# Performance work log

Measured on AMD Instinct MI355X. Metric: run time of the kernel, lower is better.

The kernel has to match this reference:

```python
import jax, jax.numpy as jnp
import numpy as np

N_NODES = 100000
N_EDGES = 1000000
IN_F, HID_F, OUT_F = 128, 128, 16


def setup_inputs() -> dict:
    key = jax.random.key(0)
    ks = jax.random.split(key, 8)
    x = jax.random.normal(ks[0], (N_NODES, IN_F), dtype=jnp.float32)
    src = jax.random.randint(ks[1], (N_EDGES,), 0, N_NODES, dtype=jnp.int64)
    dst = jax.random.randint(ks[2], (N_EDGES,), 0, N_NODES, dtype=jnp.int64)
    s = 1.0 / np.sqrt(HID_F)
    W1 = jax.random.normal(ks[3], (IN_F, HID_F), dtype=jnp.float32) * s
    W2 = jax.random.normal(ks[4], (HID_F, HID_F), dtype=jnp.float32) * s
    W3 = jax.random.normal(ks[5], (HID_F, HID_F), dtype=jnp.float32) * s
    W4 = jax.random.normal(ks[6], (HID_F, HID_F), dtype=jnp.float32) * s
    W5 = jax.random.normal(ks[7], (HID_F, OUT_F), dtype=jnp.float32) * s
    return {
        "x": x, "src": src, "dst": dst,
        "W1": W1, "b1": jnp.zeros((HID_F,), jnp.float32),
        "W2": W2, "b2": jnp.zeros((HID_F,), jnp.float32),
        "W3": W3, "b3": jnp.zeros((HID_F,), jnp.float32),
        "W4": W4, "b4": jnp.zeros((HID_F,), jnp.float32),
        "W5": W5, "b5": jnp.zeros((OUT_F,), jnp.float32),
    }


def reference(x, src, dst, W1, b1, W2, b2, W3, b3, W4, b4, W5, b5):
    N = x.shape[0]
    # in-degree per destination node (static graph, computed once)
    deg = jax.ops.segment_sum(jnp.ones_like(dst, dtype=x.dtype), dst, num_segments=N)
    inv = (1.0 / (deg + 1.0))[:, None]  # gcn aggregator normalizer: 1/(deg_in+1)

    def sage_gcn(h, W, b):
        # h_neigh[v] = (h[v] + sum_{u->v} h[u]) / (deg_in(v)+1); then linear
        agg = (h + jax.ops.segment_sum(h[src], dst, num_segments=N)) * inv
        return agg @ W + b

    h = jax.nn.relu(sage_gcn(x, W1, b1))
    h = jax.nn.relu(sage_gcn(h, W2, b2))
    h = jax.nn.relu(sage_gcn(h, W3, b3))
    h = jax.nn.relu(sage_gcn(h, W4, b4))
    h = sage_gcn(h, W5, b5)
    return jax.nn.log_softmax(h, axis=-1)
```

## Files before the change

kernel.cpp:

```cpp
#include <hip/hip_runtime.h>
#include <hip/hip_bf16.h>

#define NNODES 100000
#define NP (NNODES + 8)
#define NEDGES 1000000
#define HID 128
#define OUTF 16
#define NB 16
#define NBKT (NNODES / NB)
#define BCAP 81920
#define KB 64
#define BZT 1024
#define NSL 4

typedef __attribute__((ext_vector_type(8))) short short8;
typedef __attribute__((ext_vector_type(4))) float floatx4;
typedef __attribute__((ext_vector_type(4))) unsigned int uintx4;
typedef unsigned int uint32;
typedef unsigned long long ull;
typedef unsigned short ushort16;

__device__ __forceinline__ float blo(uint32 u) { return __uint_as_float(u << 16); }
__device__ __forceinline__ float bhi(uint32 u) { return __uint_as_float(u & 0xffff0000u); }
__device__ __forceinline__ ushort16 f2b(float f) {
    __hip_bfloat16 h = __float2bfloat16(f);
    return *reinterpret_cast<ushort16*>(&h);
}
__device__ __forceinline__ uint32 pack2(float a, float b) {
    return (uint32)f2b(a) | ((uint32)f2b(b) << 16);
}


__global__ __launch_bounds__(BZT) void bucketize(const int* __restrict__ src,
                                                 const int* __restrict__ dst,
                                                 int* __restrict__ bcursor,
                                                 ull* __restrict__ stage, int E) {
    __shared__ int cnt[NB], lbase[NB], gbase[NB];
    __shared__ int2 buf[BZT];
    __shared__ unsigned char bb[BZT];
    int t = threadIdx.x;
    int e0 = blockIdx.x * BZT;
    int e = e0 + t;
    if (t < NB) cnt[t] = 0;
    __syncthreads();
    int s = 0, d = 0, b = 0, r = 0;
    bool valid = e < E;
    if (valid) {
        s = src[e];
        d = dst[e];
        b = d / NBKT;
        r = atomicAdd(&cnt[b], 1);
    }
    __syncthreads();
    if (t == 0) {
        int run = 0;
        for (int i = 0; i < NB; i++) { lbase[i] = run; run += cnt[i]; }
    }
    __syncthreads();
    if (valid) {
        int p = lbase[b] + r;
        buf[p] = make_int2(s, d);
        bb[p] = (unsigned char)b;
    }
    if (t < NB) gbase[t] = atomicAdd(&bcursor[t], cnt[t]);
    __syncthreads();
    int nvalid = min(BZT, E - e0);
    if (t < nvalid) {
        int b2 = bb[t];
        int2 sd = buf[t];
        int pos = gbase[b2] + (t - lbase[b2]);
        if (pos < BCAP) {
            ull val = (ull)(unsigned)sd.x | ((ull)(unsigned)sd.y << 32);
            __builtin_nontemporal_store(val, &stage[(size_t)b2 * BCAP + pos]);
        }
    }
}


__global__ __launch_bounds__(256) void count_rank(const ull* __restrict__ stage,
                                                  const int* __restrict__ bcursor,
                                                  int* __restrict__ counts,
                                                  int* __restrict__ rnk) {
    int blk = blockIdx.x;
    int b = (blk & 7) + 8 * ((blk >> 3) & 1);
    int slot = blk >> 4;
    int cntb = min(bcursor[b], BCAP);
    int per = (cntb + KB - 1) / KB;
    int s0 = slot * per;
    int s1 = min(s0 + per, cntb);
    const ull* st = stage + (size_t)b * BCAP;
    int* rk = rnk + (size_t)b * BCAP;
    for (int i = s0 + threadIdx.x; i < s1; i += 256) {
        ull v = st[i];
        int d = (int)(unsigned)(v >> 32);
        rk[i] = atomicAdd(&counts[d], 1);
    }
}


__global__ __launch_bounds__(256) void fill2(const ull* __restrict__ stage,
                                             const int* __restrict__ rnk,
                                             const int* __restrict__ bcursor,
                                             const int* __restrict__ offs,
                                             int* __restrict__ csr) {
    int blk = blockIdx.x;
    int b = (blk & 7) + 8 * ((blk >> 3) & 1);
    int slot = blk >> 4;
    int cntb = min(bcursor[b], BCAP);
    int per = (cntb + KB - 1) / KB;
    int s0 = slot * per;
    int s1 = min(s0 + per, cntb);
    const ull* st = stage + (size_t)b * BCAP;
    const int* rk = rnk + (size_t)b * BCAP;
    for (int i = s0 + threadIdx.x; i < s1; i += 256) {
        ull v = st[i];
        int s = (int)(v & 0xffffffffu);
        int d = (int)(unsigned)(v >> 32);
        csr[offs[d] + rk[i]] = s;
    }
}

__global__ void scan1(const int* __restrict__ counts, int* __restrict__ offs,
                      int* __restrict__ bsum, int N) {
    __shared__ int tmp[256];
    int t = threadIdx.x;
    int i = blockIdx.x * 256 + t;
    int v = (i < N) ? ((counts[i] + 7) & ~7) : 0;
    tmp[t] = v;
    __syncthreads();
    for (int d = 1; d < 256; d <<= 1) {
        int add = (t >= d) ? tmp[t - d] : 0;
        __syncthreads();
        tmp[t] += add;
        __syncthreads();
    }
    if (i < N) offs[i] = tmp[t] - v;
    if (t == 255) bsum[blockIdx.x] = tmp[255];
}

__global__ void scan2(int* __restrict__ bsum, int nb) {
    __shared__ int tmp[512];
    int t = threadIdx.x;
    int v = (t < nb) ? bsum[t] : 0;
    tmp[t] = v;
    __syncthreads();
    for (int d = 1; d < 512; d <<= 1) {
        int add = (t >= d) ? tmp[t - d] : 0;
        __syncthreads();
        tmp[t] += add;
        __syncthreads();
    }
    if (t < nb) bsum[t] = tmp[t] - v;
}

__global__ void scan3(int* __restrict__ offs, const int* __restrict__ bsum,
                      const int* __restrict__ counts, float* __restrict__ invs,
                      int* __restrict__ csr, int N) {
    int i = blockIdx.x * 256 + threadIdx.x;
    if (i < N) {
        int o = offs[i] + bsum[blockIdx.x];
        offs[i] = o;
        int c = counts[i];
        invs[i] = 1.0f / (float)(c + 1);
        int c8 = (c + 7) & ~7;
        for (int k = c; k < c8; k++) csr[o + k] = NNODES;
    }
}


__global__ void pack_all(const float* __restrict__ W1, const float* __restrict__ W2,
                         const float* __restrict__ W3, const float* __restrict__ W4,
                         ushort16* __restrict__ Wp1, ushort16* __restrict__ Wp2,
                         ushort16* __restrict__ Wp3, ushort16* __restrict__ Wp4,
                         uint32* __restrict__ zb, uint32* __restrict__ hb,
                         uint32* __restrict__ z16b) {
    int blk = blockIdx.x;
    int lane = threadIdx.x;
    if (blk < 128) {
        int w = blk >> 5, b = blk & 31;
        const float* W = w == 0 ? W1 : w == 1 ? W2 : w == 2 ? W3 : W4;
        ushort16* Wp = w == 0 ? Wp1 : w == 1 ? Wp2 : w == 2 ? Wp3 : Wp4;
        int nt = b >> 2, ks = b & 3;
        int n = nt * 16 + (lane & 15);
        int kbase = ks * 32 + ((lane >> 4) << 3);
        ushort16 tmp[8];
#pragma unroll
        for (int i = 0; i < 8; i++) tmp[i] = f2b(W[(size_t)(kbase + i) * HID + n]);
        *(uint4*)&Wp[((size_t)b * 64 + lane) * 8] = *(uint4*)tmp;
    } else {
        for (int i = lane; i < 4 * 8 * 16; i += 64) {
            int s = i >> 7, rem = i & 127, r = rem >> 4, k = rem & 15;
            zb[((size_t)s * NP + NNODES + r) * 16 + k] = 0;
            hb[((size_t)s * NP + NNODES + r) * 16 + k] = 0;
        }
        for (int i = lane; i < 64; i += 64)
            z16b[(size_t)(NNODES + (i >> 3)) * 8 + (i & 7)] = 0;
    }
}


template <int AF32>
__global__ __launch_bounds__(256) void gemm_mfma(const void* __restrict__ Av,
                                                 const ushort16* __restrict__ Wp,
                                                 ushort16* __restrict__ Z, int M) {
    __shared__ __align__(16) ushort16 Wl[32 * 64 * 8];
    int t = threadIdx.x;
    const uint4* wp4 = (const uint4*)Wp;
    uint4* wl4 = (uint4*)Wl;
#pragma unroll
    for (int p = 0; p < 8; p++) wl4[t + p * 256] = wp4[t + p * 256];
    __syncthreads();

    int wv = t >> 6, lane = t & 63;
    int kb = (lane >> 4) << 3;
    int c4 = (lane >> 4) << 2;

    for (int rt = 0; rt < 4; rt++) {
        int row = blockIdx.x * 256 + rt * 64 + wv * 16 + (lane & 15);
        int rowc = min(row, M - 1);

        short8 a[4];
        if (AF32) {
            const float* A = (const float*)Av;
#pragma unroll
            for (int ks = 0; ks < 4; ks++) {
                const float* p = A + (size_t)rowc * HID + ks * 32 + kb;
                floatx4 lo = *(const floatx4*)p;
                floatx4 hi = *(const floatx4*)(p + 4);
                union { short8 s; ushort16 u[8]; } cv;
                cv.u[0] = f2b(lo.x); cv.u[1] = f2b(lo.y); cv.u[2] = f2b(lo.z); cv.u[3] = f2b(lo.w);
                cv.u[4] = f2b(hi.x); cv.u[5] = f2b(hi.y); cv.u[6] = f2b(hi.z); cv.u[7] = f2b(hi.w);
                a[ks] = cv.s;
            }
        } else {
            const ushort16* A = (const ushort16*)Av;
#pragma unroll
            for (int ks = 0; ks < 4; ks++)
                a[ks] = *(const short8*)(A + ((size_t)ks * NP + rowc) * 32 + kb);
        }

        floatx4 acc[8];
#pragma unroll
        for (int nt = 0; nt < 8; nt++) acc[nt] = (floatx4){0.f, 0.f, 0.f, 0.f};

#pragma unroll
        for (int nt = 0; nt < 8; nt++) {
#pragma unroll
            for (int ks = 0; ks < 4; ks++) {
                short8 w = *(const short8*)&Wl[(size_t)(((nt << 2) | ks) * 64 + lane) * 8];
                acc[nt] = __builtin_amdgcn_mfma_f32_16x16x32_bf16(w, a[ks], acc[nt], 0, 0, 0);
            }
        }

        if (row < M) {
#pragma unroll
            for (int nt = 0; nt < 8; nt++) {
                int col = nt * 16 + c4;
                int sl = col >> 5, off2 = col & 31;
                union { ushort16 u[4]; uint2 v; } pk;
                pk.u[0] = f2b(acc[nt][0]);
                pk.u[1] = f2b(acc[nt][1]);
                pk.u[2] = f2b(acc[nt][2]);
                pk.u[3] = f2b(acc[nt][3]);
                *(uint2*)&Z[((size_t)sl * NP + row) * 32 + off2] = pk.v;
            }
        }
    }
}


#define ACCN(acc0, acc1, acc2, acc3, g)                \
    {                                                  \
        acc0.x += blo((g).x); acc0.y += bhi((g).x);    \
        acc1.x += blo((g).y); acc1.y += bhi((g).y);    \
        acc2.x += blo((g).z); acc2.y += bhi((g).z);    \
        acc3.x += blo((g).w); acc3.y += bhi((g).w);    \
    }

__global__ __launch_bounds__(256) void agg_sliced(const uint32* __restrict__ Z,
                                                  const int* __restrict__ offs,
                                                  const int* __restrict__ counts,
                                                  const int* __restrict__ csr,
                                                  const float* __restrict__ invs,
                                                  const float* __restrict__ bias,
                                                  uint32* __restrict__ H, int N) {
    int s = blockIdx.x & 3;
    int chunk = blockIdx.x >> 2;
    int t = threadIdx.x;
    int l = t & 3;
    int p = chunk * 64 + (t >> 2);
    bool act = p < N;
    int pc = act ? p : N - 1;
    const uint4* Zs = (const uint4*)(Z + (size_t)s * NP * 16);
    uint4* Hs = (uint4*)(H + (size_t)s * NP * 16);

    int beg = offs[pc];
    int cnt8 = (counts[pc] + 7) & ~7;
    float sc = invs[pc];

    uint4 sv = Zs[(size_t)pc * 4 + l];
    float2 acc0 = make_float2(blo(sv.x), bhi(sv.x));
    float2 acc1 = make_float2(blo(sv.y), bhi(sv.y));
    float2 acc2 = make_float2(blo(sv.z), bhi(sv.z));
    float2 acc3 = make_float2(blo(sv.w), bhi(sv.w));

    for (int j = 0; j < cnt8; j += 8) {
        int4 ia = *(const int4*)&csr[beg + j];
        int4 ib = *(const int4*)&csr[beg + j + 4];
        uint4 g[8];
        g[0] = Zs[(size_t)ia.x * 4 + l];
        g[1] = Zs[(size_t)ia.y * 4 + l];
        g[2] = Zs[(size_t)ia.z * 4 + l];
        g[3] = Zs[(size_t)ia.w * 4 + l];
        g[4] = Zs[(size_t)ib.x * 4 + l];
        g[5] = Zs[(size_t)ib.y * 4 + l];
        g[6] = Zs[(size_t)ib.z * 4 + l];
        g[7] = Zs[(size_t)ib.w * 4 + l];
#pragma unroll
        for (int q = 0; q < 8; q++) ACCN(acc0, acc1, acc2, acc3, g[q]);
    }

    const float* bp = bias + s * 32 + l * 8;
    floatx4 b01 = *(const floatx4*)bp;
    floatx4 b23 = *(const floatx4*)(bp + 4);
    uintx4 o;
    o.x = pack2(fmaxf(acc0.x * sc + b01.x, 0.f), fmaxf(acc0.y * sc + b01.y, 0.f));
    o.y = pack2(fmaxf(acc1.x * sc + b01.z, 0.f), fmaxf(acc1.y * sc + b01.w, 0.f));
    o.z = pack2(fmaxf(acc2.x * sc + b23.x, 0.f), fmaxf(acc2.y * sc + b23.y, 0.f));
    o.w = pack2(fmaxf(acc3.x * sc + b23.z, 0.f), fmaxf(acc3.y * sc + b23.w, 0.f));
    if (act) __builtin_nontemporal_store(o, (uintx4*)&Hs[(size_t)p * 4 + l]);
}


__global__ __launch_bounds__(256) void gemm16(const uint32* __restrict__ A,
                                              const float* __restrict__ W5,
                                              uint32* __restrict__ Z16, int M) {
    __shared__ float Ws[HID * OUTF];
    int t = threadIdx.x;
    for (int i = t; i < HID * OUTF; i += 256) Ws[i] = W5[i];
    __syncthreads();
    int gid = blockIdx.x * 256 + t;
    int r = gid >> 3, cp = gid & 7;
    if (r >= M) return;
    float a0 = 0.f, a1 = 0.f;
#pragma unroll
    for (int s4 = 0; s4 < 4; s4++) {
        const uint32* ar = A + ((size_t)s4 * NP + r) * 16;
#pragma unroll
        for (int k = 0; k < 16; k++) {
            uint32 u = ar[k];
            float f0 = blo(u), f1 = bhi(u);
            a0 += f0 * Ws[(s4 * 32 + 2 * k) * OUTF + 2 * cp] +
                  f1 * Ws[(s4 * 32 + 2 * k + 1) * OUTF + 2 * cp];
            a1 += f0 * Ws[(s4 * 32 + 2 * k) * OUTF + 2 * cp + 1] +
                  f1 * Ws[(s4 * 32 + 2 * k + 1) * OUTF + 2 * cp + 1];
        }
    }
    Z16[(size_t)r * 8 + cp] = pack2(a0, a1);
}


__global__ __launch_bounds__(256) void agg16_lsm(const uint32* __restrict__ Z16,
                                                 const int* __restrict__ offs,
                                                 const int* __restrict__ counts,
                                                 const int* __restrict__ csr,
                                                 const float* __restrict__ invs,
                                                 const float* __restrict__ b5,
                                                 float* __restrict__ out, int N) {
    int t = threadIdx.x;
    int l = t & 1;
    int p = blockIdx.x * 128 + (t >> 1);
    bool act = p < N;
    int pc = act ? p : N - 1;
    const uint4* Zs = (const uint4*)Z16;

    uint4 sv = Zs[(size_t)pc * 2 + l];
    float2 acc0 = make_float2(blo(sv.x), bhi(sv.x));
    float2 acc1 = make_float2(blo(sv.y), bhi(sv.y));
    float2 acc2 = make_float2(blo(sv.z), bhi(sv.z));
    float2 acc3 = make_float2(blo(sv.w), bhi(sv.w));

    int beg = offs[pc];
    int cnt8 = (counts[pc] + 7) & ~7;
    for (int j = 0; j < cnt8; j += 8) {
        int4 ia = *(const int4*)&csr[beg + j];
        int4 ib = *(const int4*)&csr[beg + j + 4];
        uint4 g[8];
        g[0] = Zs[(size_t)ia.x * 2 + l];
        g[1] = Zs[(size_t)ia.y * 2 + l];
        g[2] = Zs[(size_t)ia.z * 2 + l];
        g[3] = Zs[(size_t)ia.w * 2 + l];
        g[4] = Zs[(size_t)ib.x * 2 + l];
        g[5] = Zs[(size_t)ib.y * 2 + l];
        g[6] = Zs[(size_t)ib.z * 2 + l];
        g[7] = Zs[(size_t)ib.w * 2 + l];
#pragma unroll
        for (int q = 0; q < 8; q++) ACCN(acc0, acc1, acc2, acc3, g[q]);
    }

    float sc = invs[pc];
    const float* bp = b5 + l * 8;
    floatx4 b01 = *(const floatx4*)bp;
    floatx4 b23 = *(const floatx4*)(bp + 4);
    float val[8];
    val[0] = acc0.x * sc + b01.x; val[1] = acc0.y * sc + b01.y;
    val[2] = acc1.x * sc + b01.z; val[3] = acc1.y * sc + b01.w;
    val[4] = acc2.x * sc + b23.x; val[5] = acc2.y * sc + b23.y;
    val[6] = acc3.x * sc + b23.z; val[7] = acc3.y * sc + b23.w;
    float mm = val[0];
#pragma unroll
    for (int k = 1; k < 8; k++) mm = fmaxf(mm, val[k]);
    mm = fmaxf(mm, __shfl_xor(mm, 1, 64));
    float ss = 0.f;
#pragma unroll
    for (int k = 0; k < 8; k++) ss += expf(val[k] - mm);
    ss += __shfl_xor(ss, 1, 64);
    float ls = mm + logf(ss);
    if (act) {
        float4 o0 = make_float4(val[0] - ls, val[1] - ls, val[2] - ls, val[3] - ls);
        float4 o1 = make_float4(val[4] - ls, val[5] - ls, val[6] - ls, val[7] - ls);
        float* op = out + (size_t)p * OUTF + l * 8;
        *(float4*)op = o0;
        *(float4*)(op + 4) = o1;
    }
}


extern "C" void kernel_launch(void* const* d_in, const int* in_sizes, int n_in,
                              void* d_out, int out_size, void* d_ws, size_t ws_size,
                              hipStream_t stream) {
    const float* x   = (const float*)d_in[0];
    const int*   src = (const int*)d_in[1];
    const int*   dst = (const int*)d_in[2];
    const float* W1 = (const float*)d_in[3];
    const float* b1 = (const float*)d_in[4];
    const float* W2 = (const float*)d_in[5];
    const float* b2 = (const float*)d_in[6];
    const float* W3 = (const float*)d_in[7];
    const float* b3 = (const float*)d_in[8];
    const float* W4 = (const float*)d_in[9];
    const float* b4 = (const float*)d_in[10];
    const float* W5 = (const float*)d_in[11];
    const float* b5 = (const float*)d_in[12];

    char* ws = (char*)d_ws;
    size_t off = 0;
    auto alloc = [&](size_t bytes) {
        void* p = ws + off;
        off = (off + bytes + 255) & ~(size_t)255;
        return p;
    };
    const size_t CSR_ELEMS = (size_t)NEDGES + 7 * (size_t)NNODES + 64;
    ushort16* zb   = (ushort16*)alloc((size_t)NSL * NP * 32 * 2);
    ushort16* hb   = (ushort16*)alloc((size_t)NSL * NP * 32 * 2);
    uint32*   z16b = (uint32*)alloc((size_t)NP * OUTF * 2);
    int*      counts = (int*)alloc((size_t)(NNODES + NB) * 4);
    int*      bcursor = counts + NNODES;
    float*    invs   = (float*)alloc((size_t)NNODES * 4);
    int*      offs   = (int*)alloc((size_t)(NNODES + 1) * 4);
    int*      bsum   = (int*)alloc(512 * 4);
    int*      csr    = (int*)alloc(CSR_ELEMS * 4);
    ull*      stage  = (ull*)alloc((size_t)NB * BCAP * 8);
    int*      rnk    = (int*)alloc((size_t)NB * BCAP * 4);
    ushort16* Wp1 = (ushort16*)alloc((size_t)HID * HID * 2);
    ushort16* Wp2 = (ushort16*)alloc((size_t)HID * HID * 2);
    ushort16* Wp3 = (ushort16*)alloc((size_t)HID * HID * 2);
    ushort16* Wp4 = (ushort16*)alloc((size_t)HID * HID * 2);
    (void)ws_size; (void)in_sizes; (void)n_in; (void)out_size;

    const int N = NNODES, E = NEDGES;
    int nb = (N + 255) / 256;

    hipMemsetAsync(counts, 0, (size_t)(NNODES + NB) * 4, stream);
    bucketize<<<(E + BZT - 1) / BZT, BZT, 0, stream>>>(src, dst, bcursor, stage, E);
    count_rank<<<NB * KB, 256, 0, stream>>>(stage, bcursor, counts, rnk);
    scan1<<<nb, 256, 0, stream>>>(counts, offs, bsum, N);
    scan2<<<1, 512, 0, stream>>>(bsum, nb);
    scan3<<<nb, 256, 0, stream>>>(offs, bsum, counts, invs, csr, N);
    fill2<<<NB * KB, 256, 0, stream>>>(stage, rnk, bcursor, offs, csr);
    pack_all<<<129, 64, 0, stream>>>(W1, W2, W3, W4, Wp1, Wp2, Wp3, Wp4,
                                     (uint32*)zb, (uint32*)hb, z16b);

    int gemmGrid = (N + 255) / 256;
    int aggGrid  = NSL * ((N + 63) / 64);
    int agg16Grid = (N + 127) / 128;

    gemm_mfma<1><<<gemmGrid, 256, 0, stream>>>((const void*)x, Wp1, zb, N);
    agg_sliced<<<aggGrid, 256, 0, stream>>>((const uint32*)zb, offs, counts, csr, invs, b1,
                                            (uint32*)hb, N);

    gemm_mfma<0><<<gemmGrid, 256, 0, stream>>>((const void*)hb, Wp2, zb, N);
    agg_sliced<<<aggGrid, 256, 0, stream>>>((const uint32*)zb, offs, counts, csr, invs, b2,
                                            (uint32*)hb, N);

    gemm_mfma<0><<<gemmGrid, 256, 0, stream>>>((const void*)hb, Wp3, zb, N);
    agg_sliced<<<aggGrid, 256, 0, stream>>>((const uint32*)zb, offs, counts, csr, invs, b3,
                                            (uint32*)hb, N);

    gemm_mfma<0><<<gemmGrid, 256, 0, stream>>>((const void*)hb, Wp4, zb, N);
    agg_sliced<<<aggGrid, 256, 0, stream>>>((const uint32*)zb, offs, counts, csr, invs, b4,
                                            (uint32*)hb, N);

    gemm16<<<(N * 8 + 255) / 256, 256, 0, stream>>>((const uint32*)hb, W5, z16b, N);
    agg16_lsm<<<agg16Grid, 256, 0, stream>>>(z16b, offs, counts, csr, invs, b5,
                                             (float*)d_out, N);
}
```

Measured before the change: 342.6 us.

## Fold rank into staged edges, merge scans into one atomic-base pass

Each edge's per-destination rank is packed into the upper bits of the staged destination word, which removes the separate rank array and its extra read and write. The three-kernel scan is replaced by a single kernel that takes each block's base offset from a global atomic cursor, cutting two launches. Nontemporal loads are also used for the edge inputs and the CSR index reads. Blocks obtain their bases in arbitrary order, so the CSR segments are no longer in node order; offsets stay consistent, but memory locality may change.

New measurement: 376.7 us. 1.1x slower.

```diff
diff --git a/kernel.cpp b/kernel.cpp
--- a/kernel.cpp
+++ b/kernel.cpp
@@ -16,6 +16,7 @@
 typedef __attribute__((ext_vector_type(8))) short short8;
 typedef __attribute__((ext_vector_type(4))) float floatx4;
 typedef __attribute__((ext_vector_type(4))) unsigned int uintx4;
+typedef __attribute__((ext_vector_type(4))) int intx4;
 typedef unsigned int uint32;
 typedef unsigned long long ull;
 typedef unsigned short ushort16;
@@ -46,8 +47,8 @@
     int s = 0, d = 0, b = 0, r = 0;
     bool valid = e < E;
     if (valid) {
-        s = src[e];
-        d = dst[e];
+        s = __builtin_nontemporal_load(&src[e]);
+        d = __builtin_nontemporal_load(&dst[e]);
         b = d / NBKT;
         r = atomicAdd(&cnt[b], 1);
     }
@@ -77,10 +78,9 @@
 }
 
 
-__global__ __launch_bounds__(256) void count_rank(const ull* __restrict__ stage,
+__global__ __launch_bounds__(256) void count_rank(ull* __restrict__ stage,
                                                   const int* __restrict__ bcursor,
-                                                  int* __restrict__ counts,
-                                                  int* __restrict__ rnk) {
+                                                  int* __restrict__ counts) {
     int blk = blockIdx.x;
     int b = (blk & 7) + 8 * ((blk >> 3) & 1);
     int slot = blk >> 4;
@@ -88,18 +88,17 @@
     int per = (cntb + KB - 1) / KB;
     int s0 = slot * per;
     int s1 = min(s0 + per, cntb);
-    const ull* st = stage + (size_t)b * BCAP;
-    int* rk = rnk + (size_t)b * BCAP;
+    uint32* st32 = (uint32*)(stage + (size_t)b * BCAP);
     for (int i = s0 + threadIdx.x; i < s1; i += 256) {
-        ull v = st[i];
-        int d = (int)(unsigned)(v >> 32);
-        rk[i] = atomicAdd(&counts[d], 1);
+        uint32 hi = st32[2 * i + 1];
+        int d = (int)(hi & 0x1ffffu);
+        int rk = atomicAdd(&counts[d], 1);
+        st32[2 * i + 1] = hi | ((uint32)rk << 17);
     }
 }
 
 
 __global__ __launch_bounds__(256) void fill2(const ull* __restrict__ stage,
-                                             const int* __restrict__ rnk,
                                              const int* __restrict__ bcursor,
                                              const int* __restrict__ offs,
                                              int* __restrict__ csr) {
@@ -111,22 +110,29 @@
     int s0 = slot * per;
     int s1 = min(s0 + per, cntb);
     const ull* st = stage + (size_t)b * BCAP;
-    const int* rk = rnk + (size_t)b * BCAP;
     for (int i = s0 + threadIdx.x; i < s1; i += 256) {
         ull v = st[i];
         int s = (int)(v & 0xffffffffu);
-        int d = (int)(unsigned)(v >> 32);
-        csr[offs[d] + rk[i]] = s;
-    }
-}
-
-__global__ void scan1(const int* __restrict__ counts, int* __restrict__ offs,
-                      int* __restrict__ bsum, int N) {
+        uint32 hi = (uint32)(v >> 32);
+        int d = (int)(hi & 0x1ffffu);
+        int r = (int)(hi >> 17);
+        csr[offs[d] + r] = s;
+    }
+}
+
+
+__global__ __launch_bounds__(256) void scan_all(const int* __restrict__ counts,
+                                                int* __restrict__ offs,
+                                                float* __restrict__ invs,
+                                                int* __restrict__ csr,
+                                                int* __restrict__ gcur, int N) {
     __shared__ int tmp[256];
+    __shared__ int base;
     int t = threadIdx.x;
     int i = blockIdx.x * 256 + t;
-    int v = (i < N) ? ((counts[i] + 7) & ~7) : 0;
-    tmp[t] = v;
+    int c = (i < N) ? counts[i] : 0;
+    int c8 = (c + 7) & ~7;
+    tmp[t] = c8;
     __syncthreads();
     for (int d = 1; d < 256; d <<= 1) {
         int add = (t >= d) ? tmp[t - d] : 0;
@@ -134,35 +140,12 @@
         tmp[t] += add;
         __syncthreads();
     }
-    if (i < N) offs[i] = tmp[t] - v;
-    if (t == 255) bsum[blockIdx.x] = tmp[255];
-}
-
-__global__ void scan2(int* __restrict__ bsum, int nb) {
-    __shared__ int tmp[512];
-    int t = threadIdx.x;
-    int v = (t < nb) ? bsum[t] : 0;
-    tmp[t] = v;
-    __syncthreads();
-    for (int d = 1; d < 512; d <<= 1) {
-        int add = (t >= d) ? tmp[t - d] : 0;
-        __syncthreads();
-        tmp[t] += add;
-        __syncthreads();
-    }
-    if (t < nb) bsum[t] = tmp[t] - v;
-}
-
-__global__ void scan3(int* __restrict__ offs, const int* __restrict__ bsum,
-                      const int* __restrict__ counts, float* __restrict__ invs,
-                      int* __restrict__ csr, int N) {
-    int i = blockIdx.x * 256 + threadIdx.x;
+    if (t == 255) base = atomicAdd(gcur, tmp[255]);
+    __syncthreads();
     if (i < N) {
-        int o = offs[i] + bsum[blockIdx.x];
+        int o = base + tmp[t] - c8;
         offs[i] = o;
-        int c = counts[i];
         invs[i] = 1.0f / (float)(c + 1);
-        int c8 = (c + 7) & ~7;
         for (int k = c; k < c8; k++) csr[o + k] = NNODES;
     }
 }
@@ -305,8 +288,8 @@
     float2 acc3 = make_float2(blo(sv.w), bhi(sv.w));
 
     for (int j = 0; j < cnt8; j += 8) {
-        int4 ia = *(const int4*)&csr[beg + j];
-        int4 ib = *(const int4*)&csr[beg + j + 4];
+        intx4 ia = __builtin_nontemporal_load((const intx4*)&csr[beg + j]);
+        intx4 ib = __builtin_nontemporal_load((const intx4*)&csr[beg + j + 4]);
         uint4 g[8];
         g[0] = Zs[(size_t)ia.x * 4 + l];
         g[1] = Zs[(size_t)ia.y * 4 + l];
@@ -383,8 +366,8 @@
     int beg = offs[pc];
     int cnt8 = (counts[pc] + 7) & ~7;
     for (int j = 0; j < cnt8; j += 8) {
-        int4 ia = *(const int4*)&csr[beg + j];
-        int4 ib = *(const int4*)&csr[beg + j + 4];
+        intx4 ia = __builtin_nontemporal_load((const intx4*)&csr[beg + j]);
+        intx4 ib = __builtin_nontemporal_load((const intx4*)&csr[beg + j + 4]);
         uint4 g[8];
         g[0] = Zs[(size_t)ia.x * 2 + l];
         g[1] = Zs[(size_t)ia.y * 2 + l];
@@ -454,14 +437,13 @@
     ushort16* zb   = (ushort16*)alloc((size_t)NSL * NP * 32 * 2);
     ushort16* hb   = (ushort16*)alloc((size_t)NSL * NP * 32 * 2);
     uint32*   z16b = (uint32*)alloc((size_t)NP * OUTF * 2);
-    int*      counts = (int*)alloc((size_t)(NNODES + NB) * 4);
+    int*      counts = (int*)alloc((size_t)(NNODES + NB + 1) * 4);
     int*      bcursor = counts + NNODES;
+    int*      gcur    = bcursor + NB;
     float*    invs   = (float*)alloc((size_t)NNODES * 4);
     int*      offs   = (int*)alloc((size_t)(NNODES + 1) * 4);
-    int*      bsum   = (int*)alloc(512 * 4);
     int*      csr    = (int*)alloc(CSR_ELEMS * 4);
     ull*      stage  = (ull*)alloc((size_t)NB * BCAP * 8);
-    int*      rnk    = (int*)alloc((size_t)NB * BCAP * 4);
     ushort16* Wp1 = (ushort16*)alloc((size_t)HID * HID * 2);
     ushort16* Wp2 = (ushort16*)alloc((size_t)HID * HID * 2);
     ushort16* Wp3 = (ushort16*)alloc((size_t)HID * HID * 2);
@@ -471,13 +453,11 @@
     const int N = NNODES, E = NEDGES;
     int nb = (N + 255) / 256;
 
-    hipMemsetAsync(counts, 0, (size_t)(NNODES + NB) * 4, stream);
+    hipMemsetAsync(counts, 0, (size_t)(NNODES + NB + 1) * 4, stream);
     bucketize<<<(E + BZT - 1) / BZT, BZT, 0, stream>>>(src, dst, bcursor, stage, E);
-    count_rank<<<NB * KB, 256, 0, stream>>>(stage, bcursor, counts, rnk);
-    scan1<<<nb, 256, 0, stream>>>(counts, offs, bsum, N);
-    scan2<<<1, 512, 0, stream>>>(bsum, nb);
-    scan3<<<nb, 256, 0, stream>>>(offs, bsum, counts, invs, csr, N);
-    fill2<<<NB * KB, 256, 0, stream>>>(stage, rnk, bcursor, offs, csr);
+    count_rank<<<NB * KB, 256, 0, stream>>>(stage, bcursor, counts);
+    scan_all<<<nb, 256, 0, stream>>>(counts, offs, invs, csr, gcur, N);
+    fill2<<<NB * KB, 256, 0, stream>>>(stage, bcursor, offs, csr);
     pack_all<<<129, 64, 0, stream>>>(W1, W2, W3, W4, Wp1, Wp2, Wp3, Wp4,
                                      (uint32*)zb, (uint32*)hb, z16b);
 
```
